# Kernel optimization log

Measured on AMD Instinct MI355X. Metric: run time of the kernel, lower is better.

## Reference

```python
import jax, jax.numpy as jnp
import numpy as np

N, E, IN, HID, OUT = 40000, 640000, 128, 512, 256


def setup_inputs() -> dict:
    key = jax.random.key(0)
    ks = jax.random.split(key, 8)
    x = jax.random.normal(ks[0], (N, IN), dtype=jnp.float32)
    edge_index = jax.random.randint(ks[1], (2, E), 0, N, dtype=jnp.int64)
    # SAGEConv params: lin_l (applied to aggregated neighbors, with bias),
    # lin_r (applied to root nodes, no bias) -- PyG defaults.
    def lin(k, fin, fout):
        return jax.random.normal(k, (fin, fout), dtype=jnp.float32) / np.sqrt(fin)
    return {
        "x": x,
        "edge_index": edge_index,
        "W1l": lin(ks[2], IN, HID),
        "b1": jnp.zeros((HID,), jnp.float32),
        "W1r": lin(ks[3], IN, HID),
        "W2l": lin(ks[4], HID, OUT),
        "b2": jnp.zeros((OUT,), jnp.float32),
        "W2r": lin(ks[5], HID, OUT),
    }


def _sage_conv(x, src, dst, Wl, b, Wr):
    n = x.shape[0]
    # gather messages from source nodes, mean-aggregate at destination
    msg = x[src]                                            # [E, F]
    agg = jax.ops.segment_sum(msg, dst, num_segments=n)     # [N, F]
    cnt = jax.ops.segment_sum(jnp.ones((src.shape[0],), x.dtype), dst,
                              num_segments=n)               # [N]
    agg = agg / jnp.maximum(cnt, 1.0)[:, None]
    # out = lin_l(mean_neighbors) + lin_r(x)
    return agg @ Wl + b + x @ Wr


def reference(x, edge_index, W1l, b1, W1r, W2l, b2, W2r):
    src, dst = edge_index[0], edge_index[1]
    h = jax.nn.relu(_sage_conv(x, src, dst, W1l, b1, W1r))
    return _sage_conv(h, src, dst, W2l, b2, W2r)
```

## Files before the change

kernel.cpp:

```cpp
#include <hip/hip_runtime.h>


#define N_NODES 40000
#define N_EDGES 640000
#define F_IN 128
#define F_HID 512
#define F_OUT 256
#define NB_SCAN 157

typedef unsigned short ushort_t;
typedef __attribute__((ext_vector_type(8))) short bf16x8;
typedef __attribute__((ext_vector_type(4))) float floatx4;

__device__ __forceinline__ ushort_t f2bf(float f) {
  union { float f; unsigned int u; } x; x.f = f;
  unsigned int r = (x.u + 0x7FFFu + ((x.u >> 16) & 1u)) >> 16;
  return (ushort_t)r;
}
__device__ __forceinline__ float bf2f(ushort_t u) {
  union { unsigned int u; float f; } x; x.u = ((unsigned int)u) << 16;
  return x.f;
}

__global__ void deg_kernel(const int* __restrict__ ei, int* __restrict__ deg) {
  int e = blockIdx.x * blockDim.x + threadIdx.x;
  if (e < N_EDGES) atomicAdd(&deg[ei[N_EDGES + e]], 1);
}

__global__ void scanA_kernel(const int* __restrict__ deg, int* __restrict__ bsum) {
  __shared__ int sdata[256];
  int i = blockIdx.x * 256 + threadIdx.x;
  sdata[threadIdx.x] = (i < N_NODES) ? deg[i] : 0;
  __syncthreads();
  #pragma unroll
  for (int off = 128; off > 0; off >>= 1) {
    if (threadIdx.x < off) sdata[threadIdx.x] += sdata[threadIdx.x + off];
    __syncthreads();
  }
  if (threadIdx.x == 0) bsum[blockIdx.x] = sdata[0];
}

__global__ void scanB_kernel(const int* __restrict__ bsum, int* __restrict__ boff) {
  __shared__ int buf[2][256];
  int tid = threadIdx.x;
  int v = (tid < NB_SCAN) ? bsum[tid] : 0;
  buf[0][tid] = v;
  __syncthreads();
  int cur = 0;
  #pragma unroll
  for (int off = 1; off < 256; off <<= 1) {
    int val = buf[cur][tid];
    if (tid >= off) val += buf[cur][tid - off];
    buf[cur ^ 1][tid] = val;
    __syncthreads();
    cur ^= 1;
  }
  if (tid < NB_SCAN) boff[tid] = buf[cur][tid] - v;
}

__global__ void scanC_kernel(const int* __restrict__ deg, const int* __restrict__ boff,
                             int* __restrict__ rowptr, int* __restrict__ cursor) {
  __shared__ int buf[2][256];
  int tid = threadIdx.x;
  int i = blockIdx.x * 256 + tid;
  int v = (i < N_NODES) ? deg[i] : 0;
  buf[0][tid] = v;
  __syncthreads();
  int cur = 0;
  #pragma unroll
  for (int off = 1; off < 256; off <<= 1) {
    int val = buf[cur][tid];
    if (tid >= off) val += buf[cur][tid - off];
    buf[cur ^ 1][tid] = val;
    __syncthreads();
    cur ^= 1;
  }
  if (i < N_NODES) {
    int ex = boff[blockIdx.x] + buf[cur][tid] - v;
    rowptr[i] = ex;
    cursor[i] = ex;
    if (i == N_NODES - 1) rowptr[N_NODES] = ex + v;
  }
}

__global__ void fill_kernel(const int* __restrict__ ei, int* __restrict__ cursor,
                            int* __restrict__ col) {
  int e = blockIdx.x * blockDim.x + threadIdx.x;
  if (e < N_EDGES) {
    int d = ei[N_EDGES + e];
    int s = ei[e];
    int pos = atomicAdd(&cursor[d], 1);
    col[pos] = s;
  }
}

__global__ void cvt_x_kernel(const float* __restrict__ x, ushort_t* __restrict__ xb) {
  int i = blockIdx.x * blockDim.x + threadIdx.x;
  const int n4 = (N_NODES * F_IN) / 4;
  if (i < n4) {
    float4 v = ((const float4*)x)[i];
    ushort4 o;
    o.x = f2bf(v.x); o.y = f2bf(v.y); o.z = f2bf(v.z); o.w = f2bf(v.w);
    ((ushort4*)xb)[i] = o;
  }
}

__global__ void wt_kernel(const float* __restrict__ W, ushort_t* __restrict__ Wt,
                          int K, int N, int rowoff, int ldt) {
  int i = blockIdx.x * blockDim.x + threadIdx.x;
  if (i < K * N) {
    int n = i / K, k = i - n * K;
    Wt[(size_t)(rowoff + n) * ldt + k] = f2bf(W[(size_t)k * N + n]);
  }
}

__global__ void biascat_kernel(const float* __restrict__ b2, float* __restrict__ bc) {
  int i = threadIdx.x + blockIdx.x * blockDim.x;
  if (i < 512) bc[i] = (i < 256) ? 0.f : b2[i - 256];
}

__global__ void agg1_kernel(const ushort_t* __restrict__ Xb, ushort_t* __restrict__ Yb,
                            const int* __restrict__ rowptr, const int* __restrict__ colidx) {
  __shared__ int cols[64];
  int n = blockIdx.x, f = threadIdx.x;
  int s = rowptr[n], e = rowptr[n + 1];
  float s0 = 0.f, s1 = 0.f;
  for (int base = s; base < e; base += 64) {
    int cnt = min(64, e - base);
    __syncthreads();
    if (f < cnt) cols[f] = colidx[base + f];
    __syncthreads();
    for (int j = 0; j < cnt; ++j) {
      unsigned int v = *(const unsigned int*)(Xb + (size_t)cols[j] * F_IN + 2 * f);
      s0 += bf2f((ushort_t)(v & 0xffffu));
      s1 += bf2f((ushort_t)(v >> 16));
    }
  }
  float inv = 1.f / fmaxf((float)(e - s), 1.f);
  unsigned int o = (unsigned int)f2bf(s0 * inv) | ((unsigned int)f2bf(s1 * inv) << 16);
  *(unsigned int*)(Yb + (size_t)n * F_IN + 2 * f) = o;
}

__global__ void agg2_kernel(const ushort_t* __restrict__ hl, const float* __restrict__ hr,
                            float* __restrict__ out,
                            const int* __restrict__ rowptr, const int* __restrict__ colidx) {
  __shared__ int cols[128];
  int n = blockIdx.x, f = threadIdx.x;
  int s = rowptr[n], e = rowptr[n + 1];
  float s0 = 0.f, s1 = 0.f;
  for (int base = s; base < e; base += 128) {
    int cnt = min(128, e - base);
    __syncthreads();
    if (f < cnt) cols[f] = colidx[base + f];
    __syncthreads();
    for (int j = 0; j < cnt; ++j) {
      unsigned int v = *(const unsigned int*)(hl + (size_t)cols[j] * F_OUT + 2 * f);
      s0 += bf2f((ushort_t)(v & 0xffffu));
      s1 += bf2f((ushort_t)(v >> 16));
    }
  }
  float inv = 1.f / fmaxf((float)(e - s), 1.f);
  float2 hrv = *(const float2*)(hr + (size_t)n * F_OUT + 2 * f);
  float2 o;
  o.x = s0 * inv + hrv.x;
  o.y = s1 * inv + hrv.y;
  *(float2*)(out + (size_t)n * F_OUT + 2 * f) = o;
}

template <bool TWOPAIR, bool RELU, bool BIAS, bool OUT_BF16, bool SPLITOUT>
__global__ __launch_bounds__(256) void gemm_mfma(
    const ushort_t* __restrict__ A0, const ushort_t* __restrict__ A1,
    const ushort_t* __restrict__ W0t, const ushort_t* __restrict__ W1t,
    const float* __restrict__ bias, float* __restrict__ Cf,
    ushort_t* __restrict__ Cb, int M, int N, int K) {
  const int BM = 128, BN = 128, BK = 32;
  __shared__ ushort_t At[BM * BK];
  __shared__ ushort_t Bt[BN * BK];
  const int tid = threadIdx.x;
  const int wave = tid >> 6, lane = tid & 63;
  const int lm = lane & 15, qk = lane >> 4;
  const int wm = wave & 1, wn = wave >> 1;
  const int bm = blockIdx.x * BM, bn = blockIdx.y * BN;
  floatx4 acc[4][4] = {};
  const int npair = TWOPAIR ? 2 : 1;
  for (int p = 0; p < npair; ++p) {
    const ushort_t* __restrict__ A = p ? A1 : A0;
    const ushort_t* __restrict__ Wt = p ? W1t : W0t;
    for (int kb = 0; kb < K; kb += BK) {
      #pragma unroll
      for (int pass = 0; pass < 2; ++pass) {
        int c = pass * 256 + wave * 64 + lane;
        int row = c >> 2, kc = c & 3;
        int ar = min(bm + row, M - 1);
        const ushort_t* ga = A + (size_t)ar * K + kb + kc * 8;
        const ushort_t* gb = Wt + (size_t)(bn + row) * K + kb + kc * 8;
        ushort_t* la = At + (size_t)(pass * 256 + wave * 64) * 8;
        ushort_t* lb = Bt + (size_t)(pass * 256 + wave * 64) * 8;
        __builtin_amdgcn_global_load_lds(
            (const __attribute__((address_space(1))) void*)ga,
            (__attribute__((address_space(3))) void*)la, 16, 0, 0);
        __builtin_amdgcn_global_load_lds(
            (const __attribute__((address_space(1))) void*)gb,
            (__attribute__((address_space(3))) void*)lb, 16, 0, 0);
      }
      __syncthreads();
      bf16x8 av[4], bv[4];
      #pragma unroll
      for (int mi = 0; mi < 4; ++mi)
        av[mi] = *(const bf16x8*)(At + (wm * 64 + mi * 16 + lm) * BK + qk * 8);
      #pragma unroll
      for (int ni = 0; ni < 4; ++ni)
        bv[ni] = *(const bf16x8*)(Bt + (wn * 64 + ni * 16 + lm) * BK + qk * 8);
      #pragma unroll
      for (int mi = 0; mi < 4; ++mi)
        #pragma unroll
        for (int ni = 0; ni < 4; ++ni)
          acc[mi][ni] = __builtin_amdgcn_mfma_f32_16x16x32_bf16(
              bv[ni], av[mi], acc[mi][ni], 0, 0, 0);
      __syncthreads();
    }
  }
  #pragma unroll
  for (int ni = 0; ni < 4; ++ni) {
    int colg = bn + wn * 64 + ni * 16 + qk * 4;
    float4 b4 = {0.f, 0.f, 0.f, 0.f};
    if (BIAS) b4 = *(const float4*)&bias[colg];
    #pragma unroll
    for (int mi = 0; mi < 4; ++mi) {
      int rowg = bm + wm * 64 + mi * 16 + lm;
      if (rowg < M) {
        float v0 = acc[mi][ni][0] + b4.x;
        float v1 = acc[mi][ni][1] + b4.y;
        float v2 = acc[mi][ni][2] + b4.z;
        float v3 = acc[mi][ni][3] + b4.w;
        if (RELU) {
          v0 = fmaxf(v0, 0.f); v1 = fmaxf(v1, 0.f);
          v2 = fmaxf(v2, 0.f); v3 = fmaxf(v3, 0.f);
        }
        if (SPLITOUT) {
          if (colg < 256) {
            ushort4 o = {f2bf(v0), f2bf(v1), f2bf(v2), f2bf(v3)};
            *(ushort4*)&Cb[(size_t)rowg * 256 + colg] = o;
          } else {
            float4 o = {v0, v1, v2, v3};
            *(float4*)&Cf[(size_t)rowg * 256 + (colg - 256)] = o;
          }
        } else if (OUT_BF16) {
          ushort4 o = {f2bf(v0), f2bf(v1), f2bf(v2), f2bf(v3)};
          *(ushort4*)&Cb[(size_t)rowg * N + colg] = o;
        } else {
          float4 o = {v0, v1, v2, v3};
          *(float4*)&Cf[(size_t)rowg * N + colg] = o;
        }
      }
    }
  }
}

extern "C" void kernel_launch(void* const* d_in, const int* in_sizes, int n_in,
                              void* d_out, int out_size, void* d_ws, size_t ws_size,
                              hipStream_t stream) {
  const float* x = (const float*)d_in[0];
  const int* ei = (const int*)d_in[1];
  const float* W1l = (const float*)d_in[2];
  const float* b1 = (const float*)d_in[3];
  const float* W1r = (const float*)d_in[4];
  const float* W2l = (const float*)d_in[5];
  const float* b2 = (const float*)d_in[6];
  const float* W2r = (const float*)d_in[7];
  float* out = (float*)d_out;

  char* ws = (char*)d_ws;
  size_t off = 0;
  auto alloc = [&](size_t bytes) {
    void* p = ws + off;
    off = (off + bytes + 255) & ~(size_t)255;
    return p;
  };
  int* deg = (int*)alloc((size_t)N_NODES * 4);
  int* rowptr = (int*)alloc((size_t)(N_NODES + 1) * 4);
  int* cursor = (int*)alloc((size_t)N_NODES * 4);
  int* col = (int*)alloc((size_t)N_EDGES * 4);
  int* bsum = (int*)alloc((size_t)NB_SCAN * 4);
  int* boff = (int*)alloc((size_t)NB_SCAN * 4);
  ushort_t* x_bf = (ushort_t*)alloc((size_t)N_NODES * F_IN * 2);
  ushort_t* aggx_bf = (ushort_t*)alloc((size_t)N_NODES * F_IN * 2);
  ushort_t* h_bf = (ushort_t*)alloc((size_t)N_NODES * F_HID * 2);
  ushort_t* hl_bf = (ushort_t*)alloc((size_t)N_NODES * F_OUT * 2);
  float* hr = (float*)alloc((size_t)N_NODES * F_OUT * 4);
  ushort_t* W1lt = (ushort_t*)alloc((size_t)F_HID * F_IN * 2);
  ushort_t* W1rt = (ushort_t*)alloc((size_t)F_HID * F_IN * 2);
  ushort_t* Wcatt = (ushort_t*)alloc((size_t)512 * F_HID * 2);
  float* biascat = (float*)alloc(512 * 4);

  hipMemsetAsync(deg, 0, (size_t)N_NODES * 4, stream);
  deg_kernel<<<(N_EDGES + 255) / 256, 256, 0, stream>>>(ei, deg);
  scanA_kernel<<<NB_SCAN, 256, 0, stream>>>(deg, bsum);
  scanB_kernel<<<1, 256, 0, stream>>>(bsum, boff);
  scanC_kernel<<<NB_SCAN, 256, 0, stream>>>(deg, boff, rowptr, cursor);
  fill_kernel<<<(N_EDGES + 255) / 256, 256, 0, stream>>>(ei, cursor, col);

  cvt_x_kernel<<<(N_NODES * F_IN / 4 + 255) / 256, 256, 0, stream>>>(x, x_bf);
  wt_kernel<<<(F_IN * F_HID + 255) / 256, 256, 0, stream>>>(W1l, W1lt, F_IN, F_HID, 0, F_IN);
  wt_kernel<<<(F_IN * F_HID + 255) / 256, 256, 0, stream>>>(W1r, W1rt, F_IN, F_HID, 0, F_IN);
  wt_kernel<<<(F_HID * F_OUT + 255) / 256, 256, 0, stream>>>(W2l, Wcatt, F_HID, F_OUT, 0, F_HID);
  wt_kernel<<<(F_HID * F_OUT + 255) / 256, 256, 0, stream>>>(W2r, Wcatt, F_HID, F_OUT, 256, F_HID);
  biascat_kernel<<<2, 256, 0, stream>>>(b2, biascat);

  agg1_kernel<<<N_NODES, 64, 0, stream>>>(x_bf, aggx_bf, rowptr, col);
  gemm_mfma<true, true, true, true, false>
      <<<dim3((N_NODES + 127) / 128, F_HID / 128), 256, 0, stream>>>(
          aggx_bf, x_bf, W1lt, W1rt, b1, nullptr, h_bf, N_NODES, F_HID, F_IN);

  gemm_mfma<false, false, true, false, true>
      <<<dim3((N_NODES + 127) / 128, 512 / 128), 256, 0, stream>>>(
          h_bf, nullptr, Wcatt, nullptr, biascat, hr, hl_bf, N_NODES, 512, F_HID);
  agg2_kernel<<<N_NODES, 128, 0, stream>>>(hl_bf, hr, out, rowptr, col);
}
```

Measured before the change: 332.0 us.

## Preload full-K A panel into LDS and concatenate layer-1 weights along K

The GEMM kernel now loads a whole 64-row A panel across the full K dimension into LDS once, then streams 256-wide B tiles, using a 64x256 block tile instead of 128x128. Layer-1 left and right weights are packed into one K-concatenated matrix so the two-pair GEMM becomes a single K=256 loop. The grid is reordered so the two column blocks sharing an A panel are adjacent. This removes repeated A reloads per K step, but the A panel is loaded synchronously without overlap and uses up to 64 KB of LDS for K=512, which limits occupancy.

```diff
diff --git a/kernel.cpp b/kernel.cpp
--- a/kernel.cpp
+++ b/kernel.cpp
@@ -106,11 +106,11 @@
 }
 
 __global__ void wt_kernel(const float* __restrict__ W, ushort_t* __restrict__ Wt,
-                          int K, int N, int rowoff, int ldt) {
+                          int K, int N, int rowoff, int koff, int ldt) {
   int i = blockIdx.x * blockDim.x + threadIdx.x;
   if (i < K * N) {
     int n = i / K, k = i - n * K;
-    Wt[(size_t)(rowoff + n) * ldt + k] = f2bf(W[(size_t)k * N + n]);
+    Wt[(size_t)(rowoff + n) * ldt + koff + k] = f2bf(W[(size_t)k * N + n]);
   }
 }
 
@@ -167,91 +167,94 @@
   *(float2*)(out + (size_t)n * F_OUT + 2 * f) = o;
 }
 
-template <bool TWOPAIR, bool RELU, bool BIAS, bool OUT_BF16, bool SPLITOUT>
+template <bool TWOPAIR, bool RELU, bool BIAS, bool OUT_BF16, bool SPLITOUT, int KT>
 __global__ __launch_bounds__(256) void gemm_mfma(
     const ushort_t* __restrict__ A0, const ushort_t* __restrict__ A1,
-    const ushort_t* __restrict__ W0t, const ushort_t* __restrict__ W1t,
-    const float* __restrict__ bias, float* __restrict__ Cf,
-    ushort_t* __restrict__ Cb, int M, int N, int K) {
-  const int BM = 128, BN = 128, BK = 32;
-  __shared__ ushort_t At[BM * BK];
+    const ushort_t* __restrict__ Wt, const float* __restrict__ bias,
+    float* __restrict__ Cf, ushort_t* __restrict__ Cb, int M) {
+  const int BM = 64, BN = 256, BK = 32;
+  const int NKC = KT / 8;
+  __shared__ ushort_t Apan[64 * KT];
   __shared__ ushort_t Bt[BN * BK];
   const int tid = threadIdx.x;
   const int wave = tid >> 6, lane = tid & 63;
   const int lm = lane & 15, qk = lane >> 4;
-  const int wm = wave & 1, wn = wave >> 1;
-  const int bm = blockIdx.x * BM, bn = blockIdx.y * BN;
+  const int bn = blockIdx.x * BN;
+  const int bm = blockIdx.y * BM;
+  const int K0 = TWOPAIR ? KT / 2 : KT;
+  const int K0c = K0 / 8;
+
+  #pragma unroll
+  for (int q = 0; q < (64 * NKC) / 256; ++q) {
+    int c = tid + q * 256;
+    int kc = c & (NKC - 1);
+    int row = c / NKC;
+    const ushort_t* src = (TWOPAIR && kc >= K0c)
+        ? A1 + (size_t)(bm + row) * K0 + (kc - K0c) * 8
+        : A0 + (size_t)(bm + row) * K0 + kc * 8;
+    bf16x8 v = *(const bf16x8*)src;
+    *(bf16x8*)(Apan + ((size_t)kc * 64 + row) * 8) = v;
+  }
+
   floatx4 acc[4][4] = {};
-  const int npair = TWOPAIR ? 2 : 1;
-  for (int p = 0; p < npair; ++p) {
-    const ushort_t* __restrict__ A = p ? A1 : A0;
-    const ushort_t* __restrict__ Wt = p ? W1t : W0t;
-    for (int kb = 0; kb < K; kb += BK) {
-      #pragma unroll
-      for (int pass = 0; pass < 2; ++pass) {
-        int c = pass * 256 + wave * 64 + lane;
-        int row = c >> 2, kc = c & 3;
-        int ar = min(bm + row, M - 1);
-        const ushort_t* ga = A + (size_t)ar * K + kb + kc * 8;
-        const ushort_t* gb = Wt + (size_t)(bn + row) * K + kb + kc * 8;
-        ushort_t* la = At + (size_t)(pass * 256 + wave * 64) * 8;
-        ushort_t* lb = Bt + (size_t)(pass * 256 + wave * 64) * 8;
-        __builtin_amdgcn_global_load_lds(
-            (const __attribute__((address_space(1))) void*)ga,
-            (__attribute__((address_space(3))) void*)la, 16, 0, 0);
-        __builtin_amdgcn_global_load_lds(
-            (const __attribute__((address_space(1))) void*)gb,
-            (__attribute__((address_space(3))) void*)lb, 16, 0, 0);
-      }
-      __syncthreads();
-      bf16x8 av[4], bv[4];
-      #pragma unroll
-      for (int mi = 0; mi < 4; ++mi)
-        av[mi] = *(const bf16x8*)(At + (wm * 64 + mi * 16 + lm) * BK + qk * 8);
+  for (int kb = 0; kb < KT; kb += BK) {
+    #pragma unroll
+    for (int q = 0; q < 4; ++q) {
+      int c = q * 256 + wave * 64 + lane;
+      int n = c >> 2, kc2 = c & 3;
+      const ushort_t* gb = Wt + (size_t)(bn + n) * KT + kb + kc2 * 8;
+      ushort_t* lb = Bt + (size_t)(q * 256 + wave * 64) * 8;
+      __builtin_amdgcn_global_load_lds(
+          (const __attribute__((address_space(1))) void*)gb,
+          (__attribute__((address_space(3))) void*)lb, 16, 0, 0);
+    }
+    __syncthreads();
+    bf16x8 av[4], bv[4];
+    #pragma unroll
+    for (int mi = 0; mi < 4; ++mi)
+      av[mi] = *(const bf16x8*)(Apan + ((size_t)(kb / 8 + qk) * 64 + mi * 16 + lm) * 8);
+    #pragma unroll
+    for (int ni = 0; ni < 4; ++ni)
+      bv[ni] = *(const bf16x8*)(Bt + (size_t)(wave * 64 + ni * 16 + lm) * 32 + qk * 8);
+    #pragma unroll
+    for (int mi = 0; mi < 4; ++mi)
       #pragma unroll
       for (int ni = 0; ni < 4; ++ni)
-        bv[ni] = *(const bf16x8*)(Bt + (wn * 64 + ni * 16 + lm) * BK + qk * 8);
-      #pragma unroll
-      for (int mi = 0; mi < 4; ++mi)
-        #pragma unroll
-        for (int ni = 0; ni < 4; ++ni)
-          acc[mi][ni] = __builtin_amdgcn_mfma_f32_16x16x32_bf16(
-              bv[ni], av[mi], acc[mi][ni], 0, 0, 0);
-      __syncthreads();
-    }
-  }
+        acc[mi][ni] = __builtin_amdgcn_mfma_f32_16x16x32_bf16(
+            bv[ni], av[mi], acc[mi][ni], 0, 0, 0);
+    __syncthreads();
+  }
+
   #pragma unroll
   for (int ni = 0; ni < 4; ++ni) {
-    int colg = bn + wn * 64 + ni * 16 + qk * 4;
+    int colg = bn + wave * 64 + ni * 16 + qk * 4;
     float4 b4 = {0.f, 0.f, 0.f, 0.f};
     if (BIAS) b4 = *(const float4*)&bias[colg];
     #pragma unroll
     for (int mi = 0; mi < 4; ++mi) {
-      int rowg = bm + wm * 64 + mi * 16 + lm;
-      if (rowg < M) {
-        float v0 = acc[mi][ni][0] + b4.x;
-        float v1 = acc[mi][ni][1] + b4.y;
-        float v2 = acc[mi][ni][2] + b4.z;
-        float v3 = acc[mi][ni][3] + b4.w;
-        if (RELU) {
-          v0 = fmaxf(v0, 0.f); v1 = fmaxf(v1, 0.f);
-          v2 = fmaxf(v2, 0.f); v3 = fmaxf(v3, 0.f);
-        }
-        if (SPLITOUT) {
-          if (colg < 256) {
-            ushort4 o = {f2bf(v0), f2bf(v1), f2bf(v2), f2bf(v3)};
-            *(ushort4*)&Cb[(size_t)rowg * 256 + colg] = o;
-          } else {
-            float4 o = {v0, v1, v2, v3};
-            *(float4*)&Cf[(size_t)rowg * 256 + (colg - 256)] = o;
-          }
-        } else if (OUT_BF16) {
+      int rowg = bm + mi * 16 + lm;
+      float v0 = acc[mi][ni][0] + b4.x;
+      float v1 = acc[mi][ni][1] + b4.y;
+      float v2 = acc[mi][ni][2] + b4.z;
+      float v3 = acc[mi][ni][3] + b4.w;
+      if (RELU) {
+        v0 = fmaxf(v0, 0.f); v1 = fmaxf(v1, 0.f);
+        v2 = fmaxf(v2, 0.f); v3 = fmaxf(v3, 0.f);
+      }
+      if (SPLITOUT) {
+        if (colg < 256) {
           ushort4 o = {f2bf(v0), f2bf(v1), f2bf(v2), f2bf(v3)};
-          *(ushort4*)&Cb[(size_t)rowg * N + colg] = o;
+          *(ushort4*)&Cb[(size_t)rowg * 256 + colg] = o;
         } else {
           float4 o = {v0, v1, v2, v3};
-          *(float4*)&Cf[(size_t)rowg * N + colg] = o;
+          *(float4*)&Cf[(size_t)rowg * 256 + (colg - 256)] = o;
         }
+      } else if (OUT_BF16) {
+        ushort4 o = {f2bf(v0), f2bf(v1), f2bf(v2), f2bf(v3)};
+        *(ushort4*)&Cb[(size_t)rowg * 512 + colg] = o;
+      } else {
+        float4 o = {v0, v1, v2, v3};
+        *(float4*)&Cf[(size_t)rowg * 512 + colg] = o;
       }
     }
   }
@@ -288,8 +291,7 @@
   ushort_t* h_bf = (ushort_t*)alloc((size_t)N_NODES * F_HID * 2);
   ushort_t* hl_bf = (ushort_t*)alloc((size_t)N_NODES * F_OUT * 2);
   float* hr = (float*)alloc((size_t)N_NODES * F_OUT * 4);
-  ushort_t* W1lt = (ushort_t*)alloc((size_t)F_HID * F_IN * 2);
-  ushort_t* W1rt = (ushort_t*)alloc((size_t)F_HID * F_IN * 2);
+  ushort_t* Wcat1t = (ushort_t*)alloc((size_t)512 * 256 * 2);
   ushort_t* Wcatt = (ushort_t*)alloc((size_t)512 * F_HID * 2);
   float* biascat = (float*)alloc(512 * 4);
 
@@ -301,19 +303,19 @@
   fill_kernel<<<(N_EDGES + 255) / 256, 256, 0, stream>>>(ei, cursor, col);
 
   cvt_x_kernel<<<(N_NODES * F_IN / 4 + 255) / 256, 256, 0, stream>>>(x, x_bf);
-  wt_kernel<<<(F_IN * F_HID + 255) / 256, 256, 0, stream>>>(W1l, W1lt, F_IN, F_HID, 0, F_IN);
-  wt_kernel<<<(F_IN * F_HID + 255) / 256, 256, 0, stream>>>(W1r, W1rt, F_IN, F_HID, 0, F_IN);
-  wt_kernel<<<(F_HID * F_OUT + 255) / 256, 256, 0, stream>>>(W2l, Wcatt, F_HID, F_OUT, 0, F_HID);
-  wt_kernel<<<(F_HID * F_OUT + 255) / 256, 256, 0, stream>>>(W2r, Wcatt, F_HID, F_OUT, 256, F_HID);
+  wt_kernel<<<(F_IN * F_HID + 255) / 256, 256, 0, stream>>>(W1l, Wcat1t, 128, 512, 0, 0, 256);
+  wt_kernel<<<(F_IN * F_HID + 255) / 256, 256, 0, stream>>>(W1r, Wcat1t, 128, 512, 0, 128, 256);
+  wt_kernel<<<(F_HID * F_OUT + 255) / 256, 256, 0, stream>>>(W2l, Wcatt, 512, 256, 0, 0, 512);
+  wt_kernel<<<(F_HID * F_OUT + 255) / 256, 256, 0, stream>>>(W2r, Wcatt, 512, 256, 256, 0, 512);
   biascat_kernel<<<2, 256, 0, stream>>>(b2, biascat);
 
   agg1_kernel<<<N_NODES, 64, 0, stream>>>(x_bf, aggx_bf, rowptr, col);
-  gemm_mfma<true, true, true, true, false>
-      <<<dim3((N_NODES + 127) / 128, F_HID / 128), 256, 0, stream>>>(
-          aggx_bf, x_bf, W1lt, W1rt, b1, nullptr, h_bf, N_NODES, F_HID, F_IN);
-
-  gemm_mfma<false, false, true, false, true>
-      <<<dim3((N_NODES + 127) / 128, 512 / 128), 256, 0, stream>>>(
-          h_bf, nullptr, Wcatt, nullptr, biascat, hr, hl_bf, N_NODES, 512, F_HID);
+  gemm_mfma<true, true, true, true, false, 256>
+      <<<dim3(2, N_NODES / 64), 256, 0, stream>>>(
+          aggx_bf, x_bf, Wcat1t, b1, nullptr, h_bf, N_NODES);
+
+  gemm_mfma<false, false, true, false, true, 512>
+      <<<dim3(2, N_NODES / 64), 256, 0, stream>>>(
+          h_bf, nullptr, Wcatt, biascat, hr, hl_bf, N_NODES);
   agg2_kernel<<<N_NODES, 128, 0, stream>>>(hl_bf, hr, out, rowptr, col);
 }
```

New measurement: 325.9 us. About the same (-1.9%).
